# Optimization experiments

Measured on AMD Instinct MI355X. Metric: run time of the kernel, lower is better.

The kernel has to match this reference:

```python
import jax, jax.numpy as jnp
import numpy as np

EPS = 0.001   # EPSILON2
T1 = 1.0
T2 = 100.0
DISC = 16     # number of discrete features
B, F, K1, K2 = 524288, 16, 16, 8


def _enforce(v):
    # Enforced autograd fn: forward = max(v, EPS), backward = identity (STE)
    return v + jax.lax.stop_gradient(jnp.maximum(v, EPS) - v)


def _soft_bin(cont, interval, i_min):
    """cont: [B,F]; interval: [F,K]; i_min: [F]. Vectorized over features/bins.
    Returns (STE one-hot out [B, F*K], kmeans_loss scalar)."""
    # bin centers = i_min + running cumsum of (enforced) gaps -> [F,K]
    centers = i_min[:, None] + jnp.cumsum(_enforce(interval), axis=1)
    d = (cont[:, :, None] - centers[None, :, :]) ** 2          # [B,F,K]
    s1 = jax.nn.softmax(-T1 * d, axis=-1)                      # kmeans softmax
    kmeans_loss = jnp.sum(jnp.mean(jnp.sum(d * s1, axis=-1), axis=0))
    s2 = jax.nn.softmax(-T2 * d, axis=-1)                      # sharp softmax
    oh = jax.nn.one_hot(jnp.argmax(s2, axis=-1), d.shape[-1], dtype=s2.dtype)
    out = s2 + jax.lax.stop_gradient(oh - s2)                  # STE one-hot
    return out.reshape(cont.shape[0], -1), kmeans_loss


def setup_inputs() -> dict:
    key = jax.random.key(0)
    k1, k2, k3 = jax.random.split(key, 3)
    x = jax.random.uniform(k1, (B, DISC + F), dtype=jnp.float32)
    interval = jax.random.uniform(k2, (F, K1), dtype=jnp.float32,
                                  minval=0.01, maxval=0.12)
    interval2 = jax.random.uniform(k3, (F, K2), dtype=jnp.float32,
                                   minval=0.02, maxval=0.2)
    i_min = jnp.zeros((F,), dtype=jnp.float32)
    return {"x": x, "interval": interval, "interval2": interval2, "i_min": i_min}


def reference(x, interval, interval2, i_min):
    x_disc, cont = x[:, :DISC], x[:, DISC:]
    out1, loss1 = _soft_bin(cont, interval, i_min)
    out2, loss2 = _soft_bin(cont, interval2, i_min)
    total_out = jnp.concatenate([x_disc, out1, out2], axis=1)  # [B, DISC+F*(K1+K2)]
    return total_out, loss1 + loss2
```

## Files before the change

### kernel.cpp

```cpp
#include <hip/hip_runtime.h>


constexpr int kB      = 524288;
constexpr int kF      = 16;
constexpr int kK1     = 16;
constexpr int kK2     = 8;
constexpr int kRowIn  = 32;
constexpr int kRowOut = 400;
constexpr float kEps  = 0.001f;
constexpr int kTPB    = 256;
constexpr int kGrid   = kB / kTPB;
constexpr int kC4     = kRowOut / 4;
constexpr int kXStride = 33;

template <int K>
__device__ __forceinline__ int soft_argmax_loss(const float* __restrict__ dd,
                                                double& lacc)
{
#pragma clang fp contract(off)
    float se = 0.f, sde = 0.f;
#pragma unroll
    for (int k = 0; k < K; ++k) {
        float e = __expf(-dd[k]);
        se += e; sde += dd[k] * e;
    }
    lacc += (double)(sde / se);

    float z[K];
#pragma unroll
    for (int k = 0; k < K; ++k) z[k] = -100.0f * dd[k];
    float m = z[0]; int kmax = 0;
#pragma unroll
    for (int k = 1; k < K; ++k) {
        if (z[k] > m) { m = z[k]; kmax = k; }
    }

    bool cand = false;
#pragma unroll
    for (int k = 0; k < K; ++k)
        cand |= (k < kmax) & (z[k] >= m - 2.4e-7f);
    if (cand) {
        float e2[K]; float ss = 0.f;
        for (int k = 0; k < K; ++k) { e2[k] = expf(z[k] - m); ss += e2[k]; }
        int km = 0; float pmax = e2[0] / ss;
        for (int k = 1; k < K; ++k) {
            float p = e2[k] / ss;
            if (p > pmax) { pmax = p; km = k; }
        }
        kmax = km;
    }
    return kmax;
}

__global__ __launch_bounds__(kTPB) void binlayer_main(
    const float* __restrict__ x,
    const float* __restrict__ interval,
    const float* __restrict__ interval2,
    const float* __restrict__ i_min,
    float* __restrict__ out,
    double* __restrict__ partial)
{
#pragma clang fp contract(off)
    __shared__ float sC1[kF][kK1];
    __shared__ float sC2[kF][kK2];
    __shared__ float sX[kTPB * kXStride];
    __shared__ unsigned char sIdx[kTPB * kF];
    __shared__ double sL[kTPB / 64];

    const int tid = threadIdx.x;

    if (tid < kF) {
        const float base = i_min[tid];
        float run = 0.f;
        for (int k = 0; k < kK1; ++k) {
            run += fmaxf(interval[tid * kK1 + k], kEps);
            sC1[tid][k] = base + run;
        }
        run = 0.f;
        for (int k = 0; k < kK2; ++k) {
            run += fmaxf(interval2[tid * kK2 + k], kEps);
            sC2[tid][k] = base + run;
        }
    }

    const long long rowBase = (long long)blockIdx.x * kTPB;

    const float4* __restrict__ xin4 = (const float4*)(x + rowBase * kRowIn);
#pragma unroll
    for (int i = 0; i < (kTPB * kRowIn / 4) / kTPB; ++i) {
        int flat = i * kTPB + tid;
        float4 v = xin4[flat];
        int r = flat >> 3, c4 = flat & 7;
        float* p = &sX[r * kXStride + c4 * 4];
        p[0] = v.x; p[1] = v.y; p[2] = v.z; p[3] = v.w;
    }
    __syncthreads();

    double lacc = 0.0;
    const float* __restrict__ myc = &sX[tid * kXStride + 16];

#pragma unroll 1
    for (int f = 0; f < kF; ++f) {
        const float c = myc[f];

        float dd1[kK1];
#pragma unroll
        for (int k = 0; k < kK1; ++k) { float t = c - sC1[f][k]; dd1[k] = t * t; }
        int k1 = soft_argmax_loss<kK1>(dd1, lacc);

        float dd2[kK2];
#pragma unroll
        for (int k = 0; k < kK2; ++k) { float t = c - sC2[f][k]; dd2[k] = t * t; }
        int k2 = soft_argmax_loss<kK2>(dd2, lacc);

        sIdx[tid * kF + f] = (unsigned char)(k1 | (k2 << 4));
    }

#pragma unroll
    for (int off = 32; off > 0; off >>= 1) lacc += __shfl_down(lacc, off);
    if ((tid & 63) == 0) sL[tid >> 6] = lacc;

    __syncthreads();

    if (tid == 0) partial[blockIdx.x] = sL[0] + sL[1] + sL[2] + sL[3];

    float4* __restrict__ o4 = (float4*)(out + rowBase * kRowOut);
#pragma unroll 1
    for (int i = 0; i < kC4; ++i) {
        unsigned idx = (unsigned)(i * kTPB + tid);
        unsigned r = idx / 100u;
        unsigned c = idx - r * 100u;
        float4 o;
        if (c < 4u) {
            const float* p = &sX[r * kXStride + c * 4u];
            o.x = p[0]; o.y = p[1]; o.z = p[2]; o.w = p[3];
        } else if (c < 68u) {
            unsigned u = c - 4u, f = u >> 2, q = (u & 3u) * 4u;
            unsigned k = sIdx[r * kF + f] & 15u;
            o.x = (k == q + 0u) ? 1.f : 0.f;
            o.y = (k == q + 1u) ? 1.f : 0.f;
            o.z = (k == q + 2u) ? 1.f : 0.f;
            o.w = (k == q + 3u) ? 1.f : 0.f;
        } else {
            unsigned u = c - 68u, f = u >> 1, q = (u & 1u) * 4u;
            unsigned k = (unsigned)(sIdx[r * kF + f]) >> 4;
            o.x = (k == q + 0u) ? 1.f : 0.f;
            o.y = (k == q + 1u) ? 1.f : 0.f;
            o.z = (k == q + 2u) ? 1.f : 0.f;
            o.w = (k == q + 3u) ? 1.f : 0.f;
        }
        o4[idx] = o;
    }
}

__global__ __launch_bounds__(256) void binlayer_finalize(
    const double* __restrict__ partial,
    float* __restrict__ out)
{
    __shared__ double sL[4];
    const int tid = threadIdx.x;
    double s = 0.0;
#pragma unroll
    for (int i = 0; i < kGrid / 256; ++i)
        s += partial[i * 256 + tid];
#pragma unroll
    for (int off = 32; off > 0; off >>= 1) s += __shfl_down(s, off);
    if ((tid & 63) == 0) sL[tid >> 6] = s;
    __syncthreads();
    if (tid == 0)
        out[(long long)kB * kRowOut] =
            (float)((sL[0] + sL[1] + sL[2] + sL[3]) * (1.0 / (double)kB));
}

extern "C" void kernel_launch(void* const* d_in, const int* in_sizes, int n_in,
                              void* d_out, int out_size, void* d_ws, size_t ws_size,
                              hipStream_t stream)
{
    const float* x    = (const float*)d_in[0];
    const float* itv1 = (const float*)d_in[1];
    const float* itv2 = (const float*)d_in[2];
    const float* imin = (const float*)d_in[3];
    float* out = (float*)d_out;
    double* partial = (double*)d_ws;

    binlayer_main<<<kGrid, kTPB, 0, stream>>>(x, itv1, itv2, imin, out, partial);
    binlayer_finalize<<<1, 256, 0, stream>>>(partial, out);
}
```

Before: 891.5 us.

## Stream discrete columns directly to output and use nontemporal stores

The discrete half of each input row is now copied straight from global memory to the output with nontemporal stores, so only the continuous features are staged in LDS (stride 17 instead of 33). The one-hot write loop covers only the 96 one-hot float4 columns per row, with the inner loop unrolled by 4 and nontemporal stores. The aims are less LDS traffic, less branching in the write loop, and less cache pollution from the large output stream. The cost is that the discrete-column stores are scattered 64-byte chunks and the one-hot rows are no longer written as one contiguous sweep.

```diff
diff --git a/kernel.cpp b/kernel.cpp
--- a/kernel.cpp
+++ b/kernel.cpp
@@ -1,5 +1,7 @@
 #include <hip/hip_runtime.h>
 
+
+typedef float vfloat4 __attribute__((ext_vector_type(4)));
 
 constexpr int kB      = 524288;
 constexpr int kF      = 16;
@@ -10,8 +12,7 @@
 constexpr float kEps  = 0.001f;
 constexpr int kTPB    = 256;
 constexpr int kGrid   = kB / kTPB;
-constexpr int kC4     = kRowOut / 4;
-constexpr int kXStride = 33;
+constexpr int kXStride = 17;
 
 template <int K>
 __device__ __forceinline__ int soft_argmax_loss(const float* __restrict__ dd,
@@ -63,7 +64,7 @@
 #pragma clang fp contract(off)
     __shared__ float sC1[kF][kK1];
     __shared__ float sC2[kF][kK2];
-    __shared__ float sX[kTPB * kXStride];
+    __shared__ float sCont[kTPB * kXStride];
     __shared__ unsigned char sIdx[kTPB * kF];
     __shared__ double sL[kTPB / 64];
 
@@ -84,20 +85,30 @@
     }
 
     const long long rowBase = (long long)blockIdx.x * kTPB;
+    const vfloat4* __restrict__ xin4 = (const vfloat4*)(x + rowBase * kRowIn);
+    vfloat4* __restrict__ o4 = (vfloat4*)(out + rowBase * kRowOut);
 
-    const float4* __restrict__ xin4 = (const float4*)(x + rowBase * kRowIn);
 #pragma unroll
-    for (int i = 0; i < (kTPB * kRowIn / 4) / kTPB; ++i) {
+    for (int i = 0; i < 4; ++i) {
         int flat = i * kTPB + tid;
-        float4 v = xin4[flat];
-        int r = flat >> 3, c4 = flat & 7;
-        float* p = &sX[r * kXStride + c4 * 4];
+        int r = flat >> 2, c = flat & 3;
+        vfloat4 v = xin4[r * 8 + 4 + c];
+        float* p = &sCont[r * kXStride + c * 4];
         p[0] = v.x; p[1] = v.y; p[2] = v.z; p[3] = v.w;
     }
+
+#pragma unroll
+    for (int i = 0; i < 4; ++i) {
+        int flat = i * kTPB + tid;
+        int r = flat >> 2, c = flat & 3;
+        vfloat4 v = xin4[r * 8 + c];
+        __builtin_nontemporal_store(v, &o4[r * 100 + c]);
+    }
+
     __syncthreads();
 
     double lacc = 0.0;
-    const float* __restrict__ myc = &sX[tid * kXStride + 16];
+    const float* __restrict__ myc = &sCont[tid * kXStride];
 
 #pragma unroll 1
     for (int f = 0; f < kF; ++f) {
@@ -124,32 +135,28 @@
 
     if (tid == 0) partial[blockIdx.x] = sL[0] + sL[1] + sL[2] + sL[3];
 
-    float4* __restrict__ o4 = (float4*)(out + rowBase * kRowOut);
-#pragma unroll 1
-    for (int i = 0; i < kC4; ++i) {
+#pragma unroll 4
+    for (int i = 0; i < 96; ++i) {
         unsigned idx = (unsigned)(i * kTPB + tid);
-        unsigned r = idx / 100u;
-        unsigned c = idx - r * 100u;
-        float4 o;
-        if (c < 4u) {
-            const float* p = &sX[r * kXStride + c * 4u];
-            o.x = p[0]; o.y = p[1]; o.z = p[2]; o.w = p[3];
-        } else if (c < 68u) {
-            unsigned u = c - 4u, f = u >> 2, q = (u & 3u) * 4u;
+        unsigned r = idx / 96u;
+        unsigned c = idx - r * 96u;
+        vfloat4 o;
+        if (c < 64u) {
+            unsigned f = c >> 2, q = (c & 3u) * 4u;
             unsigned k = sIdx[r * kF + f] & 15u;
             o.x = (k == q + 0u) ? 1.f : 0.f;
             o.y = (k == q + 1u) ? 1.f : 0.f;
             o.z = (k == q + 2u) ? 1.f : 0.f;
             o.w = (k == q + 3u) ? 1.f : 0.f;
         } else {
-            unsigned u = c - 68u, f = u >> 1, q = (u & 1u) * 4u;
+            unsigned u = c - 64u, f = u >> 1, q = (u & 1u) * 4u;
             unsigned k = (unsigned)(sIdx[r * kF + f]) >> 4;
             o.x = (k == q + 0u) ? 1.f : 0.f;
             o.y = (k == q + 1u) ? 1.f : 0.f;
             o.z = (k == q + 2u) ? 1.f : 0.f;
             o.w = (k == q + 3u) ? 1.f : 0.f;
         }
-        o4[idx] = o;
+        __builtin_nontemporal_store(o, &o4[r * 100u + 4u + c]);
     }
 }
 
```

New measurement: 908.6 us. About the same (+1.9%).
